# Kernel tuning notes

Hardware: AMD Instinct MI355X
Metric: run time of the kernel (lower is better)

Reference implementation:

```python
import jax, jax.numpy as jnp
import numpy as np

SEQ_LEN = 2048
DIM = 1024
K = 24
N_FFT = 4096  # nearest power of two >= 2*seq_len - 1


def setup_inputs() -> dict:
    key = jax.random.key(0)
    k1, k2, k3, k4 = jax.random.split(key, 4)
    x = jax.random.normal(k1, (4, SEQ_LEN, DIM), dtype=jnp.float32)
    filters = jax.random.normal(k2, (SEQ_LEN, K), dtype=jnp.float32) * 0.1
    M_inputs = jax.random.normal(k3, (DIM, DIM), dtype=jnp.float32) * (DIM ** -0.5)
    M_filters = jax.random.normal(k4, (K, DIM), dtype=jnp.float32) * (K ** -0.5)
    input_pos = jnp.arange(SEQ_LEN, dtype=jnp.int32)
    return {"x": x, "filters": filters, "M_inputs": M_inputs,
            "M_filters": M_filters, "input_pos": input_pos}


def reference(x, filters, M_inputs, M_filters, input_pos):
    # STU forward, use_approx=True, use_hankel_L=False, no flash_fft, no cache.
    B, S, D = x.shape
    # alternating sign +1,-1,+1,... along sequence
    sgn = jnp.where(jnp.arange(S) % 2 == 0, 1.0, -1.0).astype(x.dtype)[None, :, None]
    x_proj = x @ M_inputs                      # (B, S, D)
    phi_proj = filters @ M_filters             # (S, D)
    # v: (1, S, D, 1) -> rfft over seq axis with length N_FFT
    V = jnp.fft.rfft(phi_proj[None, :, :, None], n=N_FFT, axis=1)
    # U: stack [u, u*sgn] on last axis -> (B, S, D, 2)
    U = jnp.fft.rfft(jnp.stack([x_proj, x_proj * sgn], axis=-1), n=N_FFT, axis=1)
    U_conv = jnp.fft.irfft(V * U, n=N_FFT, axis=1)[:, :S]   # (B, S, D, 2)
    spectral_plus = U_conv[..., 0]
    spectral_minus = U_conv[..., 1] * sgn
    return spectral_plus + spectral_minus
```

## Files before the change

kernel.cpp:

```cpp
#include <hip/hip_runtime.h>
#include <hip/hip_bf16.h>
#include <stdint.h>
#include <stddef.h>

#define DIM 1024
#define SEQ 2048
#define KF 24

using f32x4    = __attribute__((ext_vector_type(4))) float;
using bf16x8   = __attribute__((ext_vector_type(8))) short;
using uint32x4 = __attribute__((ext_vector_type(4))) unsigned int;

__device__ __forceinline__ unsigned short f2bf(float f){
  union { float f; unsigned int i; } v; v.f = f;
  unsigned int r = v.i + 0x7FFFu + ((v.i >> 16) & 1u);
  return (unsigned short)(r >> 16);
}
__device__ __forceinline__ float dot2bf(unsigned int a, unsigned int b, float c){
  float d;
  asm("v_dot2_f32_bf16 %0, %1, %2, %3" : "=v"(d) : "v"(a), "v"(b), "v"(c));
  return d;
}
__device__ __forceinline__ unsigned vext(const uint32x4 v, int i){
  return i == 0 ? v.x : i == 1 ? v.y : i == 2 ? v.z : v.w;
}
__device__ __forceinline__ void gload_lds16(const void* g, void* l){
  __builtin_amdgcn_global_load_lds(
      (const __attribute__((address_space(1))) unsigned int*)g,
      (__attribute__((address_space(3))) unsigned int*)l, 16, 0, 0);
}
__device__ __forceinline__ uint32x4 make_srsrc(const void* base, unsigned bytes){
  uint32x4 r;
  r.x = (unsigned)(uintptr_t)base;
  r.y = (unsigned)((uintptr_t)base >> 32);
  r.z = bytes;
  r.w = 0x00020000u;
  return r;
}

__global__ void k_cvt_x(const float* __restrict__ x, unsigned short* __restrict__ xb){
  int i = blockIdx.x * 256 + threadIdx.x;
  const float4* x4 = (const float4*)x;
  float4 v = x4[i];
  ushort4 o;
  o.x = f2bf(v.x); o.y = f2bf(v.y); o.z = f2bf(v.z); o.w = f2bf(v.w);
  *(ushort4*)(xb + (size_t)i * 4) = o;
}

__global__ void k_tr_M(const float* __restrict__ Mi, unsigned short* __restrict__ MbT){
  __shared__ float tile[32][33];
  int e0 = blockIdx.y * 32, d0 = blockIdx.x * 32;
  int tx = threadIdx.x, ty = threadIdx.y;
  #pragma unroll
  for (int r = 0; r < 32; r += 8)
    tile[ty + r][tx] = Mi[(size_t)(e0 + ty + r) * DIM + d0 + tx];
  __syncthreads();
  #pragma unroll
  for (int r = 0; r < 32; r += 8)
    MbT[(size_t)(d0 + ty + r) * DIM + e0 + tx] = f2bf(tile[tx][ty + r]);
}

__global__ void k_pe(const float* __restrict__ filters, const float* __restrict__ Mf,
                     unsigned int* __restrict__ pepk2){
  int r2 = blockIdx.x * 256 + threadIdx.x;
  int d  = blockIdx.y;
  float a0 = 0.f, a1 = 0.f;
  #pragma unroll
  for (int k = 0; k < KF; ++k){
    float mf = Mf[(size_t)k * DIM + d];
    a0 += filters[(size_t)(4 * r2)     * KF + k] * mf;
    a1 += filters[(size_t)(4 * r2 + 2) * KF + k] * mf;
  }
  unsigned int lo = f2bf(2.f * a0), hi = f2bf(2.f * a1);
  pepk2[(size_t)(r2 >> 3) * 8192 + (size_t)d * 8 + (r2 & 7)] = lo | (hi << 16);
}

#define BM 128
#define BN 128
#define BKK 64
__global__ void k_gemm(const unsigned short* __restrict__ A,
                       const unsigned short* __restrict__ Bt,
                       unsigned int* __restrict__ Bg){
  __shared__ unsigned short As[BM * BKK];
  __shared__ unsigned short Bs[BN * BKK];
  int tid  = threadIdx.x;
  int lane = tid & 63, wave = tid >> 6;
  int wm = wave >> 1, wn = wave & 1;
  int trow0 = blockIdx.x * BM;
  int ncol0 = blockIdx.y * BN;

  f32x4 acc[4][4] = {};

  for (int kt = 0; kt < 1024 / BKK; ++kt){
    __syncthreads();
    #pragma unroll
    for (int g = 0; g < 4; ++g){
      int c  = wave * 4 + g;
      int mr = c * 8 + (lane >> 3);
      int u  = lane & 7;
      int su = u ^ (mr & 7);
      const unsigned short* srcA = A + (size_t)(trow0 + mr) * 1024 + kt * BKK + su * 8;
      gload_lds16(srcA, (char*)As + c * 1024);
      const unsigned short* srcB = Bt + (size_t)(ncol0 + mr) * 1024 + kt * BKK + su * 8;
      gload_lds16(srcB, (char*)Bs + c * 1024);
    }
    __syncthreads();

    bf16x8 af[4][2], bfr[4][2];
    #pragma unroll
    for (int mi = 0; mi < 4; ++mi){
      int row = wm * 64 + mi * 16 + (lane & 15);
      #pragma unroll
      for (int ks = 0; ks < 2; ++ks){
        int u = ((lane >> 4) + 4 * ks) ^ (row & 7);
        af[mi][ks] = *(const bf16x8*)((const char*)As + row * 128 + u * 16);
      }
    }
    #pragma unroll
    for (int ni = 0; ni < 4; ++ni){
      int row = wn * 64 + ni * 16 + (lane & 15);
      #pragma unroll
      for (int ks = 0; ks < 2; ++ks){
        int u = ((lane >> 4) + 4 * ks) ^ (row & 7);
        bfr[ni][ks] = *(const bf16x8*)((const char*)Bs + row * 128 + u * 16);
      }
    }
    #pragma unroll
    for (int mi = 0; mi < 4; ++mi)
      #pragma unroll
      for (int ni = 0; ni < 4; ++ni)
        #pragma unroll
        for (int ks = 0; ks < 2; ++ks)
          acc[mi][ni] = __builtin_amdgcn_mfma_f32_16x16x32_bf16(
              af[mi][ks], bfr[ni][ks], acc[mi][ni], 0, 0, 0);
  }

  unsigned short* Bh = (unsigned short*)Bg;
  #pragma unroll
  for (int mi = 0; mi < 4; ++mi)
    #pragma unroll
    for (int ni = 0; ni < 4; ++ni){
      int col = ncol0 + wn * 64 + ni * 16 + (lane & 15);
      #pragma unroll
      for (int reg = 0; reg < 4; ++reg){
        int row = trow0 + wm * 64 + mi * 16 + (lane >> 4) * 4 + reg;
        unsigned short y = f2bf(acc[mi][ni][reg]);
        int t = row & 2047, bq = row >> 11;
        int p = t & 1, j = t >> 1;
        size_t strm = ((size_t)bq * 2 + p) * 1048576;
        size_t e_lo = strm + (size_t)(j >> 2) * 4096 + (size_t)col * 4 + (j & 3);
        if (j == 0) Bg[e_lo] = (unsigned int)y;
        else        Bh[2 * e_lo] = y;
        if (j < 1023){
          int j1 = j + 1;
          size_t e_hi = strm + (size_t)(j1 >> 2) * 4096 + (size_t)col * 4 + (j1 & 3);
          Bh[2 * e_hi + 1] = y;
        }
      }
    }
}

#define BLX4(dst, so) \
  asm volatile("buffer_load_dwordx4 %0, %1, %2, %3 offen" \
               : "=v"(dst) : "v"(voff), "s"(xrsrc), "s"(so))
#define BLP4_0(dst, so) \
  asm volatile("buffer_load_dwordx4 %0, %1, %2, %3 offen" \
               : "=v"(dst) : "v"(pvoff), "s"(prsrc), "s"(so))
#define BLP4_16(dst, so) \
  asm volatile("buffer_load_dwordx4 %0, %1, %2, %3 offen offset:16" \
               : "=v"(dst) : "v"(pvoff), "s"(prsrc), "s"(so))

__device__ __forceinline__ void phase_old(const uint32x4* XBO, const uint32x4* pv,
                                          float* acc){
  #pragma unroll
  for (int q = 0; q < 8; ++q)
    #pragma unroll
    for (int m = 0; m < 32; ++m){
      int idx = m - 2 * q + 16;
      if (idx >= 2 && idx < 16)
        acc[m] = dot2bf(vext(pv[q >> 2], q & 3), vext(XBO[(idx >> 2) & 3], idx & 3),
                        acc[m]);
    }
}
__device__ __forceinline__ void phase_mid_new(const uint32x4* XBM, const uint32x4* XBN,
                                              const uint32x4* pv, float* acc){
  #pragma unroll
  for (int q = 0; q < 8; ++q)
    #pragma unroll
    for (int m = 0; m < 32; ++m){
      int idx = m - 2 * q + 16;
      if (idx >= 16){
        unsigned w = (idx < 32) ? vext(XBM[(idx >> 2) & 3], idx & 3)
                                : vext(XBN[(idx >> 2) & 3], idx & 3);
        acc[m] = dot2bf(vext(pv[q >> 2], q & 3), w, acc[m]);
      }
    }
}

#define BODY(XBO_, XBM_, XBN_, C) do{                                            \
  phase_old(XBO_, pv, acc);                                                      \
  __builtin_amdgcn_sched_barrier(0);                                             \
  { unsigned _xs = (unsigned)(4 * (C) + 4) * 16384u;                             \
    BLX4(XBO_[0], _xs);                                                          \
    BLX4(XBO_[1], _xs + 16384u);                                                 \
    BLX4(XBO_[2], _xs + 32768u);                                                 \
    BLX4(XBO_[3], _xs + 49152u);                                                 \
    unsigned _ps = pbase - 32768u * (unsigned)((C) + 1);                         \
    BLP4_0(npv[0], _ps); BLP4_16(npv[1], _ps); }                                 \
  __builtin_amdgcn_sched_barrier(0);                                             \
  phase_mid_new(XBM_, XBN_, pv, acc);                                            \
  asm volatile("s_waitcnt vmcnt(0)" ::: "memory");                               \
  __builtin_amdgcn_sched_barrier(0);                                             \
  pv[0] = npv[0]; pv[1] = npv[1];                                                \
}while(0)

__global__ __launch_bounds__(256, 4)
void k_conv(const unsigned int* __restrict__ Bg,
            const unsigned int* __restrict__ pepk2,
            float* __restrict__ out){
  int tid  = threadIdx.x;
  int bid  = blockIdx.x;
  int bp   = bid & 7;
  int rest = bid >> 3;
  int dblk = rest & 3;
  int mt   = 31 - (rest >> 2);
  int b = bp >> 1, p = bp & 1;
  int d = dblk * 256 + tid;

  uint32x4 xrsrc = make_srsrc(Bg + (size_t)bp * 1048576, 4194304u);
  uint32x4 prsrc = make_srsrc(pepk2, 2097152u);

  unsigned voff  = (unsigned)(d * 16);
  unsigned pvoff = (unsigned)(d * 32);

  uint32x4 B0[4], B1[4], B2[4], pv[2], npv[2];
  float acc[32];

  unsigned pbase = (2u * (unsigned)mt + 1u) * 32768u;
  int nch = 2 * mt + 2;

  #pragma unroll
  for (int m = 0; m < 32; ++m) acc[m] = 0.f;

  #pragma unroll
  for (int k = 0; k < 4; ++k) BLX4(B0[k], (unsigned)(k - 8) * 16384u);
  #pragma unroll
  for (int k = 0; k < 4; ++k) BLX4(B1[k], (unsigned)(k - 4) * 16384u);
  #pragma unroll
  for (int k = 0; k < 4; ++k) BLX4(B2[k], (unsigned)k * 16384u);
  BLP4_0(pv[0], pbase); BLP4_16(pv[1], pbase);
  asm volatile("s_waitcnt vmcnt(0)" ::: "memory");
  __builtin_amdgcn_sched_barrier(0);

  int c = 0;
  for (;;){
    BODY(B0, B1, B2, c); if (++c == nch) break;
    BODY(B1, B2, B0, c); if (++c == nch) break;
    BODY(B2, B0, B1, c); if (++c == nch) break;
  }

  float* oc = out + ((size_t)(b * SEQ + p) * 1024 + d) + (size_t)mt * 32 * 2048;
  #pragma unroll
  for (int m = 0; m < 32; ++m)
    __builtin_nontemporal_store(acc[m], oc + (size_t)m * 2048);
}

extern "C" void kernel_launch(void* const* d_in, const int* in_sizes, int n_in,
                              void* d_out, int out_size, void* d_ws, size_t ws_size,
                              hipStream_t stream){
  const float* x       = (const float*)d_in[0];
  const float* filters = (const float*)d_in[1];
  const float* Mi      = (const float*)d_in[2];
  const float* Mf      = (const float*)d_in[3];

  char* ws = (char*)d_ws;
  unsigned short* Xb    = (unsigned short*)(ws);
  unsigned int*   Bg    = (unsigned int*)  (ws + (size_t)16 * 1024 * 1024);
  unsigned short* MbT   = (unsigned short*)(ws + (size_t)48 * 1024 * 1024);
  unsigned int*   pepk2 = (unsigned int*)  (ws + (size_t)50 * 1024 * 1024);
  float* out = (float*)d_out;

  hipLaunchKernelGGL(k_cvt_x, dim3(8192), dim3(256), 0, stream, x, Xb);
  hipLaunchKernelGGL(k_tr_M,  dim3(32, 32), dim3(32, 8), 0, stream, Mi, MbT);
  hipLaunchKernelGGL(k_pe,    dim3(2, 1024), dim3(256), 0, stream, filters, Mf, pepk2);
  hipLaunchKernelGGL(k_gemm,  dim3(64, 8), dim3(256), 0, stream, Xb, MbT, Bg);
  hipLaunchKernelGGL(k_conv,  dim3(1024), dim3(256), 65536, stream, Bg, pepk2, out);
}
```

Before: 127.9 us.

## Store plain bf16 stream and build sliding pairs in registers with alignbit

Result: faster. 120.2 us, median of 2 (-6.1%).

```diff
diff --git a/kernel.cpp b/kernel.cpp
--- a/kernel.cpp
+++ b/kernel.cpp
@@ -21,6 +21,11 @@
   asm("v_dot2_f32_bf16 %0, %1, %2, %3" : "=v"(d) : "v"(a), "v"(b), "v"(c));
   return d;
 }
+__device__ __forceinline__ unsigned abit16(unsigned a, unsigned b){
+  unsigned d;
+  asm("v_alignbit_b32 %0, %1, %2, 16" : "=v"(d) : "v"(a), "v"(b));
+  return d;
+}
 __device__ __forceinline__ unsigned vext(const uint32x4 v, int i){
   return i == 0 ? v.x : i == 1 ? v.y : i == 2 ? v.z : v.w;
 }
@@ -28,14 +33,6 @@
   __builtin_amdgcn_global_load_lds(
       (const __attribute__((address_space(1))) unsigned int*)g,
       (__attribute__((address_space(3))) unsigned int*)l, 16, 0, 0);
-}
-__device__ __forceinline__ uint32x4 make_srsrc(const void* base, unsigned bytes){
-  uint32x4 r;
-  r.x = (unsigned)(uintptr_t)base;
-  r.y = (unsigned)((uintptr_t)base >> 32);
-  r.z = bytes;
-  r.w = 0x00020000u;
-  return r;
 }
 
 __global__ void k_cvt_x(const float* __restrict__ x, unsigned short* __restrict__ xb){
@@ -71,7 +68,7 @@
     a0 += filters[(size_t)(4 * r2)     * KF + k] * mf;
     a1 += filters[(size_t)(4 * r2 + 2) * KF + k] * mf;
   }
-  unsigned int lo = f2bf(2.f * a0), hi = f2bf(2.f * a1);
+  unsigned int lo = f2bf(2.f * a1), hi = f2bf(2.f * a0);
   pepk2[(size_t)(r2 >> 3) * 8192 + (size_t)d * 8 + (r2 & 7)] = lo | (hi << 16);
 }
 
@@ -80,7 +77,7 @@
 #define BKK 64
 __global__ void k_gemm(const unsigned short* __restrict__ A,
                        const unsigned short* __restrict__ Bt,
-                       unsigned int* __restrict__ Bg){
+                       unsigned short* __restrict__ Y8){
   __shared__ unsigned short As[BM * BKK];
   __shared__ unsigned short Bs[BN * BKK];
   int tid  = threadIdx.x;
@@ -135,7 +132,6 @@
               af[mi][ks], bfr[ni][ks], acc[mi][ni], 0, 0, 0);
   }
 
-  unsigned short* Bh = (unsigned short*)Bg;
   #pragma unroll
   for (int mi = 0; mi < 4; ++mi)
     #pragma unroll
@@ -147,30 +143,18 @@
         unsigned short y = f2bf(acc[mi][ni][reg]);
         int t = row & 2047, bq = row >> 11;
         int p = t & 1, j = t >> 1;
-        size_t strm = ((size_t)bq * 2 + p) * 1048576;
-        size_t e_lo = strm + (size_t)(j >> 2) * 4096 + (size_t)col * 4 + (j & 3);
-        if (j == 0) Bg[e_lo] = (unsigned int)y;
-        else        Bh[2 * e_lo] = y;
-        if (j < 1023){
-          int j1 = j + 1;
-          size_t e_hi = strm + (size_t)(j1 >> 2) * 4096 + (size_t)col * 4 + (j1 & 3);
-          Bh[2 * e_hi + 1] = y;
-        }
-      }
-    }
-}
-
-#define BLX4(dst, so) \
-  asm volatile("buffer_load_dwordx4 %0, %1, %2, %3 offen" \
-               : "=v"(dst) : "v"(voff), "s"(xrsrc), "s"(so))
-#define BLP4_0(dst, so) \
-  asm volatile("buffer_load_dwordx4 %0, %1, %2, %3 offen" \
-               : "=v"(dst) : "v"(pvoff), "s"(prsrc), "s"(so))
-#define BLP4_16(dst, so) \
-  asm volatile("buffer_load_dwordx4 %0, %1, %2, %3 offen offset:16" \
-               : "=v"(dst) : "v"(pvoff), "s"(prsrc), "s"(so))
-
-__device__ __forceinline__ void phase_old(const uint32x4* XBO, const uint32x4* pv,
+        size_t e = ((size_t)(bq * 2 + p)) * 1048576 +
+                   (size_t)(j >> 3) * 8192 + (size_t)col * 8 + (j & 7);
+        Y8[e] = y;
+      }
+    }
+}
+
+#define GLD4(dst, vo, base) do{ unsigned _vo = (vo);                             \
+  asm volatile("global_load_dwordx4 %0, %1, %2"                                  \
+               : "=v"(dst) : "v"(_vo), "s"(base)); }while(0)
+
+__device__ __forceinline__ void phase_old(const unsigned* PA, const uint32x4* pv,
                                           float* acc){
   #pragma unroll
   for (int q = 0; q < 8; ++q)
@@ -178,11 +162,10 @@
     for (int m = 0; m < 32; ++m){
       int idx = m - 2 * q + 16;
       if (idx >= 2 && idx < 16)
-        acc[m] = dot2bf(vext(pv[q >> 2], q & 3), vext(XBO[(idx >> 2) & 3], idx & 3),
-                        acc[m]);
-    }
-}
-__device__ __forceinline__ void phase_mid_new(const uint32x4* XBM, const uint32x4* XBN,
+        acc[m] = dot2bf(vext(pv[q >> 2], q & 3), PA[idx], acc[m]);
+    }
+}
+__device__ __forceinline__ void phase_mid_new(const unsigned* PM, const unsigned* PN,
                                               const uint32x4* pv, float* acc){
   #pragma unroll
   for (int q = 0; q < 8; ++q)
@@ -190,32 +173,46 @@
     for (int m = 0; m < 32; ++m){
       int idx = m - 2 * q + 16;
       if (idx >= 16){
-        unsigned w = (idx < 32) ? vext(XBM[(idx >> 2) & 3], idx & 3)
-                                : vext(XBN[(idx >> 2) & 3], idx & 3);
+        unsigned w = (idx < 32) ? PM[idx - 16] : PN[idx - 32];
         acc[m] = dot2bf(vext(pv[q >> 2], q & 3), w, acc[m]);
       }
     }
 }
-
-#define BODY(XBO_, XBM_, XBN_, C) do{                                            \
-  phase_old(XBO_, pv, acc);                                                      \
+__device__ __forceinline__ void build_pairs(unsigned* P, uint32x4 r0, uint32x4 r1,
+                                            unsigned& carry){
+  unsigned w0 = r0.x, w1 = r0.y, w2 = r0.z, w3 = r0.w;
+  unsigned w4 = r1.x, w5 = r1.y, w6 = r1.z, w7 = r1.w;
+  P[0]  = abit16(w0, carry); P[1]  = w0;
+  P[2]  = abit16(w1, w0);    P[3]  = w1;
+  P[4]  = abit16(w2, w1);    P[5]  = w2;
+  P[6]  = abit16(w3, w2);    P[7]  = w3;
+  P[8]  = abit16(w4, w3);    P[9]  = w4;
+  P[10] = abit16(w5, w4);    P[11] = w5;
+  P[12] = abit16(w6, w5);    P[13] = w6;
+  P[14] = abit16(w7, w6);    P[15] = w7;
+  carry = w7;
+}
+
+#define BODY(PA_, PM_, PN_, C) do{                                               \
+  phase_old(PA_, pv, acc);                                                       \
   __builtin_amdgcn_sched_barrier(0);                                             \
-  { unsigned _xs = (unsigned)(4 * (C) + 4) * 16384u;                             \
-    BLX4(XBO_[0], _xs);                                                          \
-    BLX4(XBO_[1], _xs + 16384u);                                                 \
-    BLX4(XBO_[2], _xs + 32768u);                                                 \
-    BLX4(XBO_[3], _xs + 49152u);                                                 \
-    unsigned _ps = pbase - 32768u * (unsigned)((C) + 1);                         \
-    BLP4_0(npv[0], _ps); BLP4_16(npv[1], _ps); }                                 \
+  { unsigned _g = (unsigned)(2 * ((C) + 1)) & 127u;     \
+    GLD4(r0, voff + _g * 16384u, xb);                                            \
+    GLD4(r1, voff + _g * 16384u + 16384u, xb);                                   \
+    int _pr = (int)pbase - 32768 * ((C) + 1);                                    \
+    unsigned _ps = (_pr < 0) ? 0u : (unsigned)_pr;     \
+    GLD4(npv[0], pvoff + _ps, pb);                                               \
+    GLD4(npv[1], pvoff + _ps + 16u, pb); }                                       \
   __builtin_amdgcn_sched_barrier(0);                                             \
-  phase_mid_new(XBM_, XBN_, pv, acc);                                            \
+  phase_mid_new(PM_, PN_, pv, acc);                                              \
   asm volatile("s_waitcnt vmcnt(0)" ::: "memory");                               \
   __builtin_amdgcn_sched_barrier(0);                                             \
+  build_pairs(PA_, r0, r1, carry);                                               \
   pv[0] = npv[0]; pv[1] = npv[1];                                                \
 }while(0)
 
 __global__ __launch_bounds__(256, 4)
-void k_conv(const unsigned int* __restrict__ Bg,
+void k_conv(const unsigned short* __restrict__ Y8,
             const unsigned int* __restrict__ pepk2,
             float* __restrict__ out){
   int tid  = threadIdx.x;
@@ -227,36 +224,38 @@
   int b = bp >> 1, p = bp & 1;
   int d = dblk * 256 + tid;
 
-  uint32x4 xrsrc = make_srsrc(Bg + (size_t)bp * 1048576, 4194304u);
-  uint32x4 prsrc = make_srsrc(pepk2, 2097152u);
+  const unsigned short* xb = Y8 + (size_t)bp * 1048576;
+  const unsigned int*   pb = pepk2;
 
   unsigned voff  = (unsigned)(d * 16);
   unsigned pvoff = (unsigned)(d * 32);
 
-  uint32x4 B0[4], B1[4], B2[4], pv[2], npv[2];
+  unsigned P0[16], P1[16], P2[16];
+  uint32x4 r0, r1, pv[2], npv[2];
   float acc[32];
+  unsigned carry = 0u;
 
   unsigned pbase = (2u * (unsigned)mt + 1u) * 32768u;
   int nch = 2 * mt + 2;
 
   #pragma unroll
   for (int m = 0; m < 32; ++m) acc[m] = 0.f;
-
-  #pragma unroll
-  for (int k = 0; k < 4; ++k) BLX4(B0[k], (unsigned)(k - 8) * 16384u);
-  #pragma unroll
-  for (int k = 0; k < 4; ++k) BLX4(B1[k], (unsigned)(k - 4) * 16384u);
-  #pragma unroll
-  for (int k = 0; k < 4; ++k) BLX4(B2[k], (unsigned)k * 16384u);
-  BLP4_0(pv[0], pbase); BLP4_16(pv[1], pbase);
+  #pragma unroll
+  for (int t = 0; t < 16; ++t){ P0[t] = 0u; P1[t] = 0u; }
+
+  GLD4(r0, voff, xb);
+  GLD4(r1, voff + 16384u, xb);
+  GLD4(pv[0], pvoff + pbase, pb);
+  GLD4(pv[1], pvoff + pbase + 16u, pb);
   asm volatile("s_waitcnt vmcnt(0)" ::: "memory");
   __builtin_amdgcn_sched_barrier(0);
+  build_pairs(P2, r0, r1, carry);
 
   int c = 0;
   for (;;){
-    BODY(B0, B1, B2, c); if (++c == nch) break;
-    BODY(B1, B2, B0, c); if (++c == nch) break;
-    BODY(B2, B0, B1, c); if (++c == nch) break;
+    BODY(P0, P1, P2, c); if (++c == nch) break;
+    BODY(P1, P2, P0, c); if (++c == nch) break;
+    BODY(P2, P0, P1, c); if (++c == nch) break;
   }
 
   float* oc = out + ((size_t)(b * SEQ + p) * 1024 + d) + (size_t)mt * 32 * 2048;
@@ -275,7 +274,7 @@
 
   char* ws = (char*)d_ws;
   unsigned short* Xb    = (unsigned short*)(ws);
-  unsigned int*   Bg    = (unsigned int*)  (ws + (size_t)16 * 1024 * 1024);
+  unsigned short* Y8    = (unsigned short*)(ws + (size_t)16 * 1024 * 1024);
   unsigned short* MbT   = (unsigned short*)(ws + (size_t)48 * 1024 * 1024);
   unsigned int*   pepk2 = (unsigned int*)  (ws + (size_t)50 * 1024 * 1024);
   float* out = (float*)d_out;
@@ -283,6 +282,6 @@
   hipLaunchKernelGGL(k_cvt_x, dim3(8192), dim3(256), 0, stream, x, Xb);
   hipLaunchKernelGGL(k_tr_M,  dim3(32, 32), dim3(32, 8), 0, stream, Mi, MbT);
   hipLaunchKernelGGL(k_pe,    dim3(2, 1024), dim3(256), 0, stream, filters, Mf, pepk2);
-  hipLaunchKernelGGL(k_gemm,  dim3(64, 8), dim3(256), 0, stream, Xb, MbT, Bg);
-  hipLaunchKernelGGL(k_conv,  dim3(1024), dim3(256), 65536, stream, Bg, pepk2, out);
-}
+  hipLaunchKernelGGL(k_gemm,  dim3(64, 8), dim3(256), 0, stream, Xb, MbT, Y8);
+  hipLaunchKernelGGL(k_conv,  dim3(1024), dim3(256), 65536, stream, Y8, pepk2, out);
+}
```
